# Kernel tuning notes

Hardware: AMD Instinct MI355X
Metric: run time of the kernel (lower is better)

The kernel has to match this reference:

```python
import jax, jax.numpy as jnp
import numpy as np
from jax import lax

D_MODEL = 128   # n_channels
OUT_C   = 128   # out_channels
D_STATE = 16
EXPAND  = 2
D_INNER = EXPAND * D_MODEL  # 256
D_CONV  = 4
DT_RANK = (D_MODEL + 15) // 16  # 8
LN_EPS  = 1e-5


def setup_inputs() -> dict:
    key = jax.random.key(0)
    ks = jax.random.split(key, 8)
    s = lambda k, shape: jax.random.normal(k, shape, jnp.float32) * 0.02
    return {
        "x1": jax.random.normal(ks[0], (2, D_MODEL, 64, 64), jnp.float32),
        "W_in": s(ks[1], (D_MODEL, 2 * D_INNER)),              # in_proj (no bias)
        "conv_w": s(ks[2], (D_INNER, 1, D_CONV)),              # depthwise conv kernel (O, I/g, K)
        "conv_b": jnp.zeros((D_INNER,), jnp.float32),
        "W_x": s(ks[3], (D_INNER, DT_RANK + 2 * D_STATE)),     # x_proj (no bias)
        "W_dt": s(ks[4], (DT_RANK, D_INNER)),                  # dt_proj
        "b_dt": s(ks[5], (D_INNER,)),
        "A_log": jnp.log(jnp.broadcast_to(
            jnp.arange(1, D_STATE + 1, dtype=jnp.float32), (D_INNER, D_STATE))),
        "D": jnp.ones((D_INNER,), jnp.float32),
        "W_out": s(ks[6], (D_INNER, OUT_C)),                   # out_proj (no bias)
        "ln_g": jnp.ones((OUT_C,), jnp.float32),
        "ln_b": jnp.zeros((OUT_C,), jnp.float32),
    }


def _mamba(x, W_in, conv_w, conv_b, W_x, W_dt, b_dt, A_log, D, W_out):
    # x: (b, L, d_model)
    b, L, _ = x.shape
    xz = x @ W_in                               # (b, L, 2*d_inner)
    xin, z = jnp.split(xz, 2, axis=-1)
    # causal depthwise conv1d over L
    xp = jnp.pad(xin, ((0, 0), (D_CONV - 1, 0), (0, 0)))
    xc = lax.conv_general_dilated(
        xp, conv_w, window_strides=(1,), padding='VALID',
        dimension_numbers=('NLC', 'OIL', 'NLC'),
        feature_group_count=D_INNER)
    xc = jax.nn.silu(xc + conv_b)               # (b, L, d_inner)
    # input-dependent SSM params
    xdbl = xc @ W_x                             # (b, L, dt_rank + 2*d_state)
    dt, Bm, Cm = jnp.split(xdbl, [DT_RANK, DT_RANK + D_STATE], axis=-1)
    dt = jax.nn.softplus(dt @ W_dt + b_dt)      # (b, L, d_inner)
    A = -jnp.exp(A_log)                         # (d_inner, d_state)
    dA = jnp.exp(dt[..., None] * A)                             # (b, L, d_inner, d_state)
    dBu = dt[..., None] * Bm[:, :, None, :] * xc[..., None]     # (b, L, d_inner, d_state)

    def step(h, inp):
        dA_t, dBu_t, C_t = inp                  # (b,d,s), (b,d,s), (b,s)
        h = dA_t * h + dBu_t
        y = jnp.einsum('bds,bs->bd', h, C_t)
        return h, y

    h0 = jnp.zeros((b, D_INNER, D_STATE), xc.dtype)
    _, ys = lax.scan(step, h0, (dA.transpose(1, 0, 2, 3),
                                dBu.transpose(1, 0, 2, 3),
                                Cm.transpose(1, 0, 2)))
    y = ys.transpose(1, 0, 2) + xc * D          # (b, L, d_inner)
    y = y * jax.nn.silu(z)                      # gated
    return y @ W_out                            # (b, L, out_c)


def reference(x1, W_in, conv_w, conv_b, W_x, W_dt, b_dt, A_log, D, W_out, ln_g, ln_b):
    b, c, h, w = x1.shape
    x = x1.transpose(0, 2, 3, 1).reshape(b, h * w, c)
    y = _mamba(x, W_in, conv_w, conv_b, W_x, W_dt, b_dt, A_log, D, W_out)
    mu = y.mean(-1, keepdims=True)
    var = ((y - mu) ** 2).mean(-1, keepdims=True)
    y = (y - mu) * lax.rsqrt(var + LN_EPS) * ln_g + ln_b
    return y.reshape(b, h, w, OUT_C).transpose(0, 3, 1, 2)
```

## Files before the change

kernel.cpp:

```cpp
#include <hip/hip_runtime.h>
#include <math.h>

#define B_ 2
#define DMODEL 128
#define DIN 256
#define DSTATE 16
#define DTR 8
#define OUTC 128
#define Lseq 4096
#define NC 256
#define LC 16

__device__ __forceinline__ float siluf(float x){ return x / (1.f + __expf(-x)); }

__global__ __launch_bounds__(256) void k_inproj(const float* __restrict__ x1,
        const float* __restrict__ Win, float* __restrict__ xin, float* __restrict__ zs){
    __shared__ float xt[16*DMODEL];
    int blk = blockIdx.x;
    int b = blk >> 8;
    int l0 = (blk & 255) * 16;
    int t = threadIdx.x;
    const float* xb = x1 + (size_t)b * DMODEL * Lseq;
    #pragma unroll
    for (int i = 0; i < 8; ++i){
        int e = t + i*256;
        int c = e >> 4, p = e & 15;
        xt[e] = xb[(size_t)c*Lseq + l0 + p];
    }
    __syncthreads();
    float acc0[16], acc1[16];
    #pragma unroll
    for (int p=0;p<16;++p){acc0[p]=0.f;acc1[p]=0.f;}
    for (int k=0;k<DMODEL;++k){
        float w0 = Win[k*512 + t];
        float w1 = Win[k*512 + t + 256];
        #pragma unroll
        for (int p=0;p<16;++p){
            float xv = xt[k*16 + p];
            acc0[p] = fmaf(xv, w0, acc0[p]);
            acc1[p] = fmaf(xv, w1, acc1[p]);
        }
    }
    #pragma unroll
    for (int p=0;p<16;++p){
        size_t base = ((size_t)(b*Lseq + l0 + p))*DIN;
        xin[base + t] = acc0[p];
        zs[base + t]  = siluf(acc1[p]);
    }
}

__global__ __launch_bounds__(256) void k_conv_scan1(const float* __restrict__ xin,
        const float* __restrict__ convw, const float* __restrict__ convb,
        const float* __restrict__ Wx, const float* __restrict__ Wdt,
        const float* __restrict__ bdt, const float* __restrict__ Alog,
        float* __restrict__ xc, float* __restrict__ dt,
        float* __restrict__ Bm, float* __restrict__ Cm, float2* __restrict__ PSw){
    __shared__ float xcs[32*257];
    __shared__ float xdbl[32*40];
    int blk = blockIdx.x;
    int b  = blk >> 7;
    int cb = blk & 127;
    int l0 = cb << 5;
    int t  = threadIdx.x;

    float w0 = convw[t*4+0], w1 = convw[t*4+1], w2 = convw[t*4+2], w3 = convw[t*4+3];
    float bb = convb[t];
    const float* xinb = xin + ((size_t)(b*Lseq + l0))*DIN + t;
    float x3, x2, x1;
    if (l0 == 0) { x3 = x2 = x1 = 0.f; }
    else { x3 = xinb[-3*DIN]; x2 = xinb[-2*DIN]; x1 = xinb[-1*DIN]; }
    float* xcg = xc + ((size_t)(b*Lseq + l0))*DIN + t;
    #pragma unroll 4
    for (int l = 0; l < 32; ++l){
        float x0 = xinb[l*DIN];
        float acc = bb;
        acc = fmaf(x3, w0, acc);
        acc = fmaf(x2, w1, acc);
        acc = fmaf(x1, w2, acc);
        acc = fmaf(x0, w3, acc);
        float v = siluf(acc);
        xcs[l*257 + t] = v;
        xcg[l*DIN] = v;
        x3 = x2; x2 = x1; x1 = x0;
    }
    __syncthreads();

    {
        int jg = t & 7;
        int lg = t >> 3;
        int j0 = jg * 5;
        float a0=0.f, a1=0.f, a2=0.f, a3=0.f, a4=0.f;
        const float* xrow = xcs + lg*257;
        const float* wbase = Wx + j0;
        #pragma unroll 8
        for (int d = 0; d < 256; ++d){
            float xv = xrow[d];
            const float* wr = wbase + d*40;
            a0 = fmaf(xv, wr[0], a0);
            a1 = fmaf(xv, wr[1], a1);
            a2 = fmaf(xv, wr[2], a2);
            a3 = fmaf(xv, wr[3], a3);
            a4 = fmaf(xv, wr[4], a4);
        }
        float* xo = xdbl + lg*40 + j0;
        xo[0]=a0; xo[1]=a1; xo[2]=a2; xo[3]=a3; xo[4]=a4;
    }
    __syncthreads();

    {
        float wd[DTR];
        #pragma unroll
        for (int r=0;r<DTR;++r) wd[r] = Wdt[r*DIN + t];
        float bv = bdt[t];
        float Av[16];
        {
            const float4* Ap = (const float4*)(Alog + t*DSTATE);
            #pragma unroll
            for (int q=0;q<4;++q){
                float4 a = Ap[q];
                Av[q*4]   = -__expf(a.x);
                Av[q*4+1] = -__expf(a.y);
                Av[q*4+2] = -__expf(a.z);
                Av[q*4+3] = -__expf(a.w);
            }
        }
        float P[16], S[16];
        #pragma unroll
        for (int s=0;s<16;++s){ P[s]=1.f; S[s]=0.f; }
        float* dtg = dt + ((size_t)(b*Lseq + l0))*DIN + t;
        #pragma unroll 4
        for (int l=0;l<32;++l){
            float a = bv;
            #pragma unroll
            for (int r=0;r<DTR;++r) a = fmaf(xdbl[l*40 + r], wd[r], a);
            float dtv = (a > 20.f) ? a : log1pf(__expf(a));
            dtg[l*DIN] = dtv;
            float xcv = xcs[l*257 + t];
            float dx  = dtv*xcv;
            const float4* Bv = (const float4*)&xdbl[l*40 + DTR];
            float4 B0 = Bv[0], B1 = Bv[1], B2 = Bv[2], B3 = Bv[3];
            #define ST1(i, bval) { float dA = __expf(dtv*Av[i]); P[i] *= dA; S[i] = fmaf(dA, S[i], dx*(bval)); }
            ST1(0,B0.x) ST1(1,B0.y) ST1(2,B0.z) ST1(3,B0.w)
            ST1(4,B1.x) ST1(5,B1.y) ST1(6,B1.z) ST1(7,B1.w)
            ST1(8,B2.x) ST1(9,B2.y) ST1(10,B2.z) ST1(11,B2.w)
            ST1(12,B3.x) ST1(13,B3.y) ST1(14,B3.z) ST1(15,B3.w)
            #undef ST1
            if (l == 15){
                float2* ps = PSw + ((size_t)(b*NC + cb*2))*4096 + t*DSTATE;
                #pragma unroll
                for (int s=0;s<16;++s){ ps[s] = make_float2(P[s], S[s]); P[s]=1.f; S[s]=0.f; }
            }
        }
        float2* ps = PSw + ((size_t)(b*NC + cb*2 + 1))*4096 + t*DSTATE;
        #pragma unroll
        for (int s=0;s<16;++s) ps[s] = make_float2(P[s], S[s]);
    }
    for (int o = t; o < 1024; o += 256){
        int l = o >> 5, q = o & 31;
        float v = xdbl[l*40 + DTR + q];
        size_t g = ((size_t)(b*Lseq + l0 + l))*DSTATE;
        if (q < DSTATE) Bm[g + q] = v;
        else            Cm[g + (q - DSTATE)] = v;
    }
}

__global__ __launch_bounds__(256) void k_scan2(const float2* __restrict__ PSw,
        float* __restrict__ Iw){
    int g = blockIdx.x*256 + threadIdx.x;
    int b = g >> 12;
    int r = g & 4095;
    float H = 0.f;
    #pragma unroll 8
    for (int c=0;c<NC;++c){
        size_t idx = ((size_t)(b*NC + c))*4096 + r;
        float2 ps = PSw[idx];
        Iw[idx] = H;
        H = fmaf(ps.x, H, ps.y);
    }
}

__global__ __launch_bounds__(256) void k_scan3out(const float* __restrict__ dt,
        const float* __restrict__ xc, const float* __restrict__ zs,
        const float* __restrict__ Bm, const float* __restrict__ Cm,
        const float* __restrict__ Alog, const float* __restrict__ Dv,
        const float* __restrict__ Iw,
        const float* __restrict__ Wout, const float* __restrict__ lng,
        const float* __restrict__ lnb, float* __restrict__ out){
    __shared__ float ysm[256*18];
    __shared__ float os[128*18];
    __shared__ float Bs[LC*DSTATE];
    __shared__ float Cs[LC*DSTATE];
    int blk = blockIdx.x;
    int b = blk >> 8, c = blk & 255;
    int l0 = c * LC;
    int t = threadIdx.x;
    size_t gb = (size_t)(b*Lseq + l0);
    Bs[t] = Bm[gb*DSTATE + t];
    Cs[t] = Cm[gb*DSTATE + t];
    float Av[16];
    {
        const float4* Ap = (const float4*)(Alog + t*DSTATE);
        #pragma unroll
        for (int q=0;q<4;++q){
            float4 a = Ap[q];
            Av[q*4]   = -__expf(a.x);
            Av[q*4+1] = -__expf(a.y);
            Av[q*4+2] = -__expf(a.z);
            Av[q*4+3] = -__expf(a.w);
        }
    }
    float h[16];
    {
        const float4* Ip = (const float4*)(Iw + ((size_t)(b*NC + c))*4096 + t*DSTATE);
        #pragma unroll
        for (int q=0;q<4;++q){
            float4 v = Ip[q];
            h[q*4]=v.x; h[q*4+1]=v.y; h[q*4+2]=v.z; h[q*4+3]=v.w;
        }
    }
    float Dd = Dv[t];
    float dtv[LC], xcv[LC], zvv[LC];
    {
        const float* dtp = dt + gb*DIN + t;
        const float* xcp = xc + gb*DIN + t;
        const float* zsp = zs + gb*DIN + t;
        #pragma unroll
        for (int l=0;l<LC;++l){
            dtv[l] = dtp[l*DIN];
            xcv[l] = xcp[l*DIN];
            zvv[l] = zsp[l*DIN];
        }
    }
    __syncthreads();
    #pragma unroll
    for (int l=0;l<LC;++l){
        float dtl = dtv[l];
        float dx  = dtl*xcv[l];
        const float4* Bv = (const float4*)&Bs[l*DSTATE];
        const float4* Cv = (const float4*)&Cs[l*DSTATE];
        float4 B0 = Bv[0], B1 = Bv[1], B2 = Bv[2], B3 = Bv[3];
        float4 C0 = Cv[0], C1 = Cv[1], C2 = Cv[2], C3 = Cv[3];
        float y = 0.f;
        #define ST3(i, bval, cval) { float dA = __expf(dtl*Av[i]); h[i] = fmaf(dA, h[i], dx*(bval)); y = fmaf(h[i], (cval), y); }
        ST3(0,B0.x,C0.x) ST3(1,B0.y,C0.y) ST3(2,B0.z,C0.z) ST3(3,B0.w,C0.w)
        ST3(4,B1.x,C1.x) ST3(5,B1.y,C1.y) ST3(6,B1.z,C1.z) ST3(7,B1.w,C1.w)
        ST3(8,B2.x,C2.x) ST3(9,B2.y,C2.y) ST3(10,B2.z,C2.z) ST3(11,B2.w,C2.w)
        ST3(12,B3.x,C3.x) ST3(13,B3.y,C3.y) ST3(14,B3.z,C3.z) ST3(15,B3.w,C3.w)
        #undef ST3
        ysm[t*18 + l] = (y + Dd*xcv[l])*zvv[l];
    }
    __syncthreads();
    int lg = t >> 5, cg = t & 31;
    int l0t = lg*2, c0 = cg*4;
    float acc[2][4];
    #pragma unroll
    for (int i=0;i<2;++i)
        #pragma unroll
        for (int j=0;j<4;++j) acc[i][j]=0.f;
    #pragma unroll 4
    for (int k=0;k<DIN;++k){
        float2 yv = *(const float2*)&ysm[k*18 + l0t];
        float4 wv = *(const float4*)&Wout[k*OUTC + c0];
        acc[0][0]=fmaf(yv.x,wv.x,acc[0][0]); acc[0][1]=fmaf(yv.x,wv.y,acc[0][1]);
        acc[0][2]=fmaf(yv.x,wv.z,acc[0][2]); acc[0][3]=fmaf(yv.x,wv.w,acc[0][3]);
        acc[1][0]=fmaf(yv.y,wv.x,acc[1][0]); acc[1][1]=fmaf(yv.y,wv.y,acc[1][1]);
        acc[1][2]=fmaf(yv.y,wv.z,acc[1][2]); acc[1][3]=fmaf(yv.y,wv.w,acc[1][3]);
    }
    float4 gm = *(const float4*)&lng[c0];
    float4 bt = *(const float4*)&lnb[c0];
    #pragma unroll
    for (int i=0;i<2;++i){
        float rs = acc[i][0]+acc[i][1]+acc[i][2]+acc[i][3];
        #pragma unroll
        for (int m=16;m>0;m>>=1) rs += __shfl_xor(rs, m, 64);
        float mu = rs * (1.f/128.f);
        float d0 = acc[i][0]-mu, d1 = acc[i][1]-mu, d2 = acc[i][2]-mu, d3 = acc[i][3]-mu;
        float sq = d0*d0+d1*d1+d2*d2+d3*d3;
        #pragma unroll
        for (int m=16;m>0;m>>=1) sq += __shfl_xor(sq, m, 64);
        float rstd = rsqrtf(sq * (1.f/128.f) + 1e-5f);
        int lidx = l0t + i;
        os[(c0+0)*18 + lidx] = d0*rstd*gm.x + bt.x;
        os[(c0+1)*18 + lidx] = d1*rstd*gm.y + bt.y;
        os[(c0+2)*18 + lidx] = d2*rstd*gm.z + bt.z;
        os[(c0+3)*18 + lidx] = d3*rstd*gm.w + bt.w;
    }
    __syncthreads();
    {
        int cc = t >> 1, sel = t & 1;
        const float* ip = &os[cc*18 + sel*8];
        float2 a0 = *(const float2*)(ip);
        float2 a1 = *(const float2*)(ip+2);
        float2 a2 = *(const float2*)(ip+4);
        float2 a3 = *(const float2*)(ip+6);
        float* op = out + ((size_t)(b*OUTC + cc))*Lseq + l0 + sel*8;
        *(float4*)(op)   = make_float4(a0.x,a0.y,a1.x,a1.y);
        *(float4*)(op+4) = make_float4(a2.x,a2.y,a3.x,a3.y);
    }
}

extern "C" void kernel_launch(void* const* d_in, const int* in_sizes, int n_in,
                              void* d_out, int out_size, void* d_ws, size_t ws_size,
                              hipStream_t stream) {
    const float* x1    = (const float*)d_in[0];
    const float* Win   = (const float*)d_in[1];
    const float* convw = (const float*)d_in[2];
    const float* convb = (const float*)d_in[3];
    const float* Wx    = (const float*)d_in[4];
    const float* Wdt   = (const float*)d_in[5];
    const float* bdt   = (const float*)d_in[6];
    const float* Alog  = (const float*)d_in[7];
    const float* Dv    = (const float*)d_in[8];
    const float* Wout  = (const float*)d_in[9];
    const float* lng   = (const float*)d_in[10];
    const float* lnb   = (const float*)d_in[11];
    float* out = (float*)d_out;

    float* ws  = (float*)d_ws;
    float* xin = ws;
    float* zs  = xin + 2097152;
    float* xc  = zs  + 2097152;
    float* dt  = xc  + 2097152;
    float* Bm  = dt  + 2097152;
    float* Cm  = Bm  + 131072;
    float2* PSw = (float2*)(Cm + 131072);
    float* Iw  = xin;

    k_inproj    <<<512,  256, 0, stream>>>(x1, Win, xin, zs);
    k_conv_scan1<<<256,  256, 0, stream>>>(xin, convw, convb, Wx, Wdt, bdt, Alog,
                                           xc, dt, Bm, Cm, PSw);
    k_scan2     <<<32,   256, 0, stream>>>(PSw, Iw);
    k_scan3out  <<<512,  256, 0, stream>>>(dt, xc, zs, Bm, Cm, Alog, Dv, Iw,
                                           Wout, lng, lnb, out);
}
```

Baseline: 190.5 us.

## Pack dt/xc/z into interleaved buffer, halve chunk size, split in_proj and x_proj work

Intermediate dt, xc and silu(z) are stored interleaved as float4 per channel so the output kernel reads them with one vector load, and B/C are stored per chunk contiguously. The scan chunk length drops from 16 to 8 (512 chunks), and in_proj and conv/scan1 grids double to 1024 blocks: in_proj now splits the x and z halves across blocks, and x_proj reduces over four K-slices with a shared-memory partial sum. This raises parallelism and coalescing, at the cost of double the chunk-state traffic in scan2 (the serial chain doubles), a padded float4 layout that wastes a quarter of the packed buffer's bandwidth, and a re-read of x1 by both halves in in_proj.

Result: slower. 258.6 us (+35.7%).

```diff
diff --git a/kernel.cpp b/kernel.cpp
--- a/kernel.cpp
+++ b/kernel.cpp
@@ -8,17 +8,20 @@
 #define DTR 8
 #define OUTC 128
 #define Lseq 4096
-#define NC 256
-#define LC 16
+#define NC 512
+#define LC 8
 
 __device__ __forceinline__ float siluf(float x){ return x / (1.f + __expf(-x)); }
 
-__global__ __launch_bounds__(256) void k_inproj(const float* __restrict__ x1,
-        const float* __restrict__ Win, float* __restrict__ xin, float* __restrict__ zs){
+
+__global__ __launch_bounds__(256, 4) void k_inproj(const float* __restrict__ x1,
+        const float* __restrict__ Win, float* __restrict__ xin, float* __restrict__ pk){
     __shared__ float xt[16*DMODEL];
     int blk = blockIdx.x;
-    int b = blk >> 8;
-    int l0 = (blk & 255) * 16;
+    int b  = blk >> 9;
+    int ch = (blk >> 8) & 1;
+    int lc = blk & 255;
+    int l0 = lc * 16;
     int t = threadIdx.x;
     const float* xb = x1 + (size_t)b * DMODEL * Lseq;
     #pragma unroll
@@ -28,89 +31,93 @@
         xt[e] = xb[(size_t)c*Lseq + l0 + p];
     }
     __syncthreads();
-    float acc0[16], acc1[16];
-    #pragma unroll
-    for (int p=0;p<16;++p){acc0[p]=0.f;acc1[p]=0.f;}
+    float acc[16];
+    #pragma unroll
+    for (int p=0;p<16;++p) acc[p]=0.f;
+    const float* wcol = Win + ch*256 + t;
     for (int k=0;k<DMODEL;++k){
-        float w0 = Win[k*512 + t];
-        float w1 = Win[k*512 + t + 256];
-        #pragma unroll
-        for (int p=0;p<16;++p){
-            float xv = xt[k*16 + p];
-            acc0[p] = fmaf(xv, w0, acc0[p]);
-            acc1[p] = fmaf(xv, w1, acc1[p]);
-        }
-    }
-    #pragma unroll
-    for (int p=0;p<16;++p){
-        size_t base = ((size_t)(b*Lseq + l0 + p))*DIN;
-        xin[base + t] = acc0[p];
-        zs[base + t]  = siluf(acc1[p]);
-    }
-}
-
-__global__ __launch_bounds__(256) void k_conv_scan1(const float* __restrict__ xin,
+        float w = wcol[k*512];
+        #pragma unroll
+        for (int p=0;p<16;++p) acc[p] = fmaf(xt[k*16 + p], w, acc[p]);
+    }
+    if (ch == 0){
+        #pragma unroll
+        for (int p=0;p<16;++p)
+            xin[((size_t)(b*Lseq + l0 + p))*DIN + t] = acc[p];
+    } else {
+        #pragma unroll
+        for (int p=0;p<16;++p)
+            pk[((size_t)(b*Lseq + l0 + p))*1024 + t*4 + 2] = siluf(acc[p]);
+    }
+}
+
+__global__ __launch_bounds__(256, 4) void k_conv_scan1(const float* __restrict__ xin,
         const float* __restrict__ convw, const float* __restrict__ convb,
         const float* __restrict__ Wx, const float* __restrict__ Wdt,
         const float* __restrict__ bdt, const float* __restrict__ Alog,
-        float* __restrict__ xc, float* __restrict__ dt,
-        float* __restrict__ Bm, float* __restrict__ Cm, float2* __restrict__ PSw){
-    __shared__ float xcs[32*257];
-    __shared__ float xdbl[32*40];
+        float* __restrict__ pk, float* __restrict__ BCp, float2* __restrict__ PSw){
+    __shared__ float xcs[LC*257];
+    __shared__ float part[4*LC*40];
+    __shared__ float xdbl[LC*40];
     int blk = blockIdx.x;
-    int b  = blk >> 7;
-    int cb = blk & 127;
-    int l0 = cb << 5;
-    int t  = threadIdx.x;
+    int b = blk >> 9, c = blk & 511;
+    int l0 = c * LC;
+    int t = threadIdx.x;
 
     float w0 = convw[t*4+0], w1 = convw[t*4+1], w2 = convw[t*4+2], w3 = convw[t*4+3];
     float bb = convb[t];
     const float* xinb = xin + ((size_t)(b*Lseq + l0))*DIN + t;
-    float x3, x2, x1;
-    if (l0 == 0) { x3 = x2 = x1 = 0.f; }
-    else { x3 = xinb[-3*DIN]; x2 = xinb[-2*DIN]; x1 = xinb[-1*DIN]; }
-    float* xcg = xc + ((size_t)(b*Lseq + l0))*DIN + t;
-    #pragma unroll 4
-    for (int l = 0; l < 32; ++l){
-        float x0 = xinb[l*DIN];
+    float r[11];
+    if (l0 == 0){ r[0]=r[1]=r[2]=0.f; }
+    else {
+        r[0] = xinb[-3*DIN]; r[1] = xinb[-2*DIN]; r[2] = xinb[-1*DIN];
+    }
+    #pragma unroll
+    for (int i=0;i<8;++i) r[3+i] = xinb[i*DIN];
+    float* pkb = pk + ((size_t)(b*Lseq + l0))*1024 + t*4;
+    #pragma unroll
+    for (int l=0;l<LC;++l){
         float acc = bb;
-        acc = fmaf(x3, w0, acc);
-        acc = fmaf(x2, w1, acc);
-        acc = fmaf(x1, w2, acc);
-        acc = fmaf(x0, w3, acc);
+        acc = fmaf(r[l],   w0, acc);
+        acc = fmaf(r[l+1], w1, acc);
+        acc = fmaf(r[l+2], w2, acc);
+        acc = fmaf(r[l+3], w3, acc);
         float v = siluf(acc);
         xcs[l*257 + t] = v;
-        xcg[l*DIN] = v;
-        x3 = x2; x2 = x1; x1 = x0;
-    }
-    __syncthreads();
-
-    {
+        pkb[l*1024 + 1] = v;
+    }
+    __syncthreads();
+
+    {
+        int dq = t >> 6;
+        int lg = (t >> 3) & 7;
         int jg = t & 7;
-        int lg = t >> 3;
         int j0 = jg * 5;
         float a0=0.f, a1=0.f, a2=0.f, a3=0.f, a4=0.f;
-        const float* xrow = xcs + lg*257;
-        const float* wbase = Wx + j0;
+        const float* xrow = xcs + lg*257 + dq*64;
+        const float* wbase = Wx + (size_t)dq*64*40 + j0;
         #pragma unroll 8
-        for (int d = 0; d < 256; ++d){
-            float xv = xrow[d];
-            const float* wr = wbase + d*40;
+        for (int dd = 0; dd < 64; ++dd){
+            float xv = xrow[dd];
+            const float* wr = wbase + dd*40;
             a0 = fmaf(xv, wr[0], a0);
             a1 = fmaf(xv, wr[1], a1);
             a2 = fmaf(xv, wr[2], a2);
             a3 = fmaf(xv, wr[3], a3);
             a4 = fmaf(xv, wr[4], a4);
         }
-        float* xo = xdbl + lg*40 + j0;
-        xo[0]=a0; xo[1]=a1; xo[2]=a2; xo[3]=a3; xo[4]=a4;
-    }
+        float* po = part + dq*320 + lg*40 + j0;
+        po[0]=a0; po[1]=a1; po[2]=a2; po[3]=a3; po[4]=a4;
+    }
+    __syncthreads();
+    for (int o = t; o < 320; o += 256)
+        xdbl[o] = part[o] + part[320+o] + part[640+o] + part[960+o];
     __syncthreads();
 
     {
         float wd[DTR];
         #pragma unroll
-        for (int r=0;r<DTR;++r) wd[r] = Wdt[r*DIN + t];
+        for (int rr=0;rr<DTR;++rr) wd[rr] = Wdt[rr*DIN + t];
         float bv = bdt[t];
         float Av[16];
         {
@@ -127,14 +134,13 @@
         float P[16], S[16];
         #pragma unroll
         for (int s=0;s<16;++s){ P[s]=1.f; S[s]=0.f; }
-        float* dtg = dt + ((size_t)(b*Lseq + l0))*DIN + t;
-        #pragma unroll 4
-        for (int l=0;l<32;++l){
+        #pragma unroll
+        for (int l=0;l<LC;++l){
             float a = bv;
             #pragma unroll
-            for (int r=0;r<DTR;++r) a = fmaf(xdbl[l*40 + r], wd[r], a);
+            for (int rr=0;rr<DTR;++rr) a = fmaf(xdbl[l*40 + rr], wd[rr], a);
             float dtv = (a > 20.f) ? a : log1pf(__expf(a));
-            dtg[l*DIN] = dtv;
+            pkb[l*1024 + 0] = dtv;
             float xcv = xcs[l*257 + t];
             float dx  = dtv*xcv;
             const float4* Bv = (const float4*)&xdbl[l*40 + DTR];
@@ -145,26 +151,18 @@
             ST1(8,B2.x) ST1(9,B2.y) ST1(10,B2.z) ST1(11,B2.w)
             ST1(12,B3.x) ST1(13,B3.y) ST1(14,B3.z) ST1(15,B3.w)
             #undef ST1
-            if (l == 15){
-                float2* ps = PSw + ((size_t)(b*NC + cb*2))*4096 + t*DSTATE;
-                #pragma unroll
-                for (int s=0;s<16;++s){ ps[s] = make_float2(P[s], S[s]); P[s]=1.f; S[s]=0.f; }
-            }
-        }
-        float2* ps = PSw + ((size_t)(b*NC + cb*2 + 1))*4096 + t*DSTATE;
+        }
+        float2* ps = PSw + ((size_t)(b*NC + c))*4096 + t*DSTATE;
         #pragma unroll
         for (int s=0;s<16;++s) ps[s] = make_float2(P[s], S[s]);
     }
-    for (int o = t; o < 1024; o += 256){
-        int l = o >> 5, q = o & 31;
-        float v = xdbl[l*40 + DTR + q];
-        size_t g = ((size_t)(b*Lseq + l0 + l))*DSTATE;
-        if (q < DSTATE) Bm[g + q] = v;
-        else            Cm[g + (q - DSTATE)] = v;
-    }
-}
-
-__global__ __launch_bounds__(256) void k_scan2(const float2* __restrict__ PSw,
+    {
+        int l = t >> 5, q = t & 31;
+        BCp[((size_t)(b*NC + c))*256 + t] = xdbl[l*40 + DTR + q];
+    }
+}
+
+__global__ __launch_bounds__(256, 4) void k_scan2(const float2* __restrict__ PSw,
         float* __restrict__ Iw){
     int g = blockIdx.x*256 + threadIdx.x;
     int b = g >> 12;
@@ -179,24 +177,19 @@
     }
 }
 
-__global__ __launch_bounds__(256) void k_scan3out(const float* __restrict__ dt,
-        const float* __restrict__ xc, const float* __restrict__ zs,
-        const float* __restrict__ Bm, const float* __restrict__ Cm,
-        const float* __restrict__ Alog, const float* __restrict__ Dv,
-        const float* __restrict__ Iw,
+__global__ __launch_bounds__(256, 4) void k_scan3out(const float* __restrict__ pk,
+        const float* __restrict__ BCp, const float* __restrict__ Alog,
+        const float* __restrict__ Dv, const float* __restrict__ Iw,
         const float* __restrict__ Wout, const float* __restrict__ lng,
         const float* __restrict__ lnb, float* __restrict__ out){
-    __shared__ float ysm[256*18];
-    __shared__ float os[128*18];
-    __shared__ float Bs[LC*DSTATE];
-    __shared__ float Cs[LC*DSTATE];
+    __shared__ float ysm[256*9 + 8];
+    __shared__ float os[128*9 + 8];
+    __shared__ float bc[256];
     int blk = blockIdx.x;
-    int b = blk >> 8, c = blk & 255;
+    int b = blk >> 9, c = blk & 511;
     int l0 = c * LC;
     int t = threadIdx.x;
-    size_t gb = (size_t)(b*Lseq + l0);
-    Bs[t] = Bm[gb*DSTATE + t];
-    Cs[t] = Cm[gb*DSTATE + t];
+    bc[t] = BCp[((size_t)(b*NC + c))*256 + t];
     float Av[16];
     {
         const float4* Ap = (const float4*)(Alog + t*DSTATE);
@@ -218,26 +211,20 @@
             h[q*4]=v.x; h[q*4+1]=v.y; h[q*4+2]=v.z; h[q*4+3]=v.w;
         }
     }
+    float4 trio[LC];
+    {
+        const float4* pkb = (const float4*)(pk + ((size_t)(b*Lseq + l0))*1024 + t*4);
+        #pragma unroll
+        for (int l=0;l<LC;++l) trio[l] = pkb[l*256];
+    }
     float Dd = Dv[t];
-    float dtv[LC], xcv[LC], zvv[LC];
-    {
-        const float* dtp = dt + gb*DIN + t;
-        const float* xcp = xc + gb*DIN + t;
-        const float* zsp = zs + gb*DIN + t;
-        #pragma unroll
-        for (int l=0;l<LC;++l){
-            dtv[l] = dtp[l*DIN];
-            xcv[l] = xcp[l*DIN];
-            zvv[l] = zsp[l*DIN];
-        }
-    }
     __syncthreads();
     #pragma unroll
     for (int l=0;l<LC;++l){
-        float dtl = dtv[l];
-        float dx  = dtl*xcv[l];
-        const float4* Bv = (const float4*)&Bs[l*DSTATE];
-        const float4* Cv = (const float4*)&Cs[l*DSTATE];
+        float dtl = trio[l].x, xcv = trio[l].y, zv = trio[l].z;
+        float dx  = dtl*xcv;
+        const float4* Bv = (const float4*)&bc[l*32];
+        const float4* Cv = (const float4*)&bc[l*32 + 16];
         float4 B0 = Bv[0], B1 = Bv[1], B2 = Bv[2], B3 = Bv[3];
         float4 C0 = Cv[0], C1 = Cv[1], C2 = Cv[2], C3 = Cv[3];
         float y = 0.f;
@@ -247,55 +234,45 @@
         ST3(8,B2.x,C2.x) ST3(9,B2.y,C2.y) ST3(10,B2.z,C2.z) ST3(11,B2.w,C2.w)
         ST3(12,B3.x,C3.x) ST3(13,B3.y,C3.y) ST3(14,B3.z,C3.z) ST3(15,B3.w,C3.w)
         #undef ST3
-        ysm[t*18 + l] = (y + Dd*xcv[l])*zvv[l];
+        ysm[t*9 + l] = (y + Dd*xcv)*zv;
     }
     __syncthreads();
     int lg = t >> 5, cg = t & 31;
-    int l0t = lg*2, c0 = cg*4;
-    float acc[2][4];
-    #pragma unroll
-    for (int i=0;i<2;++i)
-        #pragma unroll
-        for (int j=0;j<4;++j) acc[i][j]=0.f;
-    #pragma unroll 4
+    int c0 = cg*4;
+    float a0=0.f, a1=0.f, a2=0.f, a3=0.f;
+    #pragma unroll 8
     for (int k=0;k<DIN;++k){
-        float2 yv = *(const float2*)&ysm[k*18 + l0t];
+        float yv = ysm[k*9 + lg];
         float4 wv = *(const float4*)&Wout[k*OUTC + c0];
-        acc[0][0]=fmaf(yv.x,wv.x,acc[0][0]); acc[0][1]=fmaf(yv.x,wv.y,acc[0][1]);
-        acc[0][2]=fmaf(yv.x,wv.z,acc[0][2]); acc[0][3]=fmaf(yv.x,wv.w,acc[0][3]);
-        acc[1][0]=fmaf(yv.y,wv.x,acc[1][0]); acc[1][1]=fmaf(yv.y,wv.y,acc[1][1]);
-        acc[1][2]=fmaf(yv.y,wv.z,acc[1][2]); acc[1][3]=fmaf(yv.y,wv.w,acc[1][3]);
+        a0 = fmaf(yv, wv.x, a0);
+        a1 = fmaf(yv, wv.y, a1);
+        a2 = fmaf(yv, wv.z, a2);
+        a3 = fmaf(yv, wv.w, a3);
     }
     float4 gm = *(const float4*)&lng[c0];
     float4 bt = *(const float4*)&lnb[c0];
-    #pragma unroll
-    for (int i=0;i<2;++i){
-        float rs = acc[i][0]+acc[i][1]+acc[i][2]+acc[i][3];
+    {
+        float rs = a0+a1+a2+a3;
         #pragma unroll
         for (int m=16;m>0;m>>=1) rs += __shfl_xor(rs, m, 64);
         float mu = rs * (1.f/128.f);
-        float d0 = acc[i][0]-mu, d1 = acc[i][1]-mu, d2 = acc[i][2]-mu, d3 = acc[i][3]-mu;
+        float d0 = a0-mu, d1 = a1-mu, d2 = a2-mu, d3 = a3-mu;
         float sq = d0*d0+d1*d1+d2*d2+d3*d3;
         #pragma unroll
         for (int m=16;m>0;m>>=1) sq += __shfl_xor(sq, m, 64);
         float rstd = rsqrtf(sq * (1.f/128.f) + 1e-5f);
-        int lidx = l0t + i;
-        os[(c0+0)*18 + lidx] = d0*rstd*gm.x + bt.x;
-        os[(c0+1)*18 + lidx] = d1*rstd*gm.y + bt.y;
-        os[(c0+2)*18 + lidx] = d2*rstd*gm.z + bt.z;
-        os[(c0+3)*18 + lidx] = d3*rstd*gm.w + bt.w;
+        os[(c0+0)*9 + lg] = d0*rstd*gm.x + bt.x;
+        os[(c0+1)*9 + lg] = d1*rstd*gm.y + bt.y;
+        os[(c0+2)*9 + lg] = d2*rstd*gm.z + bt.z;
+        os[(c0+3)*9 + lg] = d3*rstd*gm.w + bt.w;
     }
     __syncthreads();
     {
         int cc = t >> 1, sel = t & 1;
-        const float* ip = &os[cc*18 + sel*8];
-        float2 a0 = *(const float2*)(ip);
-        float2 a1 = *(const float2*)(ip+2);
-        float2 a2 = *(const float2*)(ip+4);
-        float2 a3 = *(const float2*)(ip+6);
-        float* op = out + ((size_t)(b*OUTC + cc))*Lseq + l0 + sel*8;
-        *(float4*)(op)   = make_float4(a0.x,a0.y,a1.x,a1.y);
-        *(float4*)(op+4) = make_float4(a2.x,a2.y,a3.x,a3.y);
+        const float* ip = &os[cc*9 + sel*4];
+        float v0 = ip[0], v1 = ip[1], v2 = ip[2], v3 = ip[3];
+        float* op = out + ((size_t)(b*OUTC + cc))*Lseq + l0 + sel*4;
+        *(float4*)op = make_float4(v0, v1, v2, v3);
     }
 }
 
@@ -318,18 +295,15 @@
 
     float* ws  = (float*)d_ws;
     float* xin = ws;
-    float* zs  = xin + 2097152;
-    float* xc  = zs  + 2097152;
-    float* dt  = xc  + 2097152;
-    float* Bm  = dt  + 2097152;
-    float* Cm  = Bm  + 131072;
-    float2* PSw = (float2*)(Cm + 131072);
-    float* Iw  = xin;
-
-    k_inproj    <<<512,  256, 0, stream>>>(x1, Win, xin, zs);
-    k_conv_scan1<<<256,  256, 0, stream>>>(xin, convw, convb, Wx, Wdt, bdt, Alog,
-                                           xc, dt, Bm, Cm, PSw);
+    float* pk  = xin + 2097152;
+    float2* PSw = (float2*)(pk + 8388608);
+    float* Iw  = (float*)(PSw + 4194304);
+    float* BCp = Iw + 4194304;
+
+    k_inproj    <<<1024, 256, 0, stream>>>(x1, Win, xin, pk);
+    k_conv_scan1<<<1024, 256, 0, stream>>>(xin, convw, convb, Wx, Wdt, bdt, Alog,
+                                           pk, BCp, PSw);
     k_scan2     <<<32,   256, 0, stream>>>(PSw, Iw);
-    k_scan3out  <<<512,  256, 0, stream>>>(dt, xc, zs, Bm, Cm, Alog, Dv, Iw,
+    k_scan3out  <<<1024, 256, 0, stream>>>(pk, BCp, Alog, Dv, Iw,
                                            Wout, lng, lnb, out);
 }
```
